# Kernel optimization log

Measured on AMD Instinct MI355X. Metric: run time of the kernel, lower is better.

## Reference

```python
import jax, jax.numpy as jnp
import numpy as np

N = 20        # number_of_nodes
K = 2         # Chebyshev order
E_DIM = 4     # embedding_dimensions
OUT = 2       # out_channels
F_IN = 8      # node_features
B = 131072    # batch


def setup_inputs() -> dict:
    key = jax.random.key(0)
    ks = jax.random.split(key, 8)
    x = jax.random.normal(ks[0], (B, N, F_IN), jnp.float32)
    e = jax.random.normal(ks[1], (N, E_DIM), jnp.float32)
    # AVWGCN parameter pools: weights_pool (E_DIM, K, in, out), bias_pool (E_DIM, out)
    gate_w = jax.random.normal(ks[2], (E_DIM, K, F_IN + OUT, 2 * OUT), jnp.float32) * 0.1
    gate_b = jax.random.normal(ks[3], (E_DIM, 2 * OUT), jnp.float32) * 0.1
    upd_w = jax.random.normal(ks[4], (E_DIM, K, F_IN + OUT, OUT), jnp.float32) * 0.1
    upd_b = jax.random.normal(ks[5], (E_DIM, OUT), jnp.float32) * 0.1
    lin_w = jax.random.normal(ks[6], (1, OUT), jnp.float32) * 0.5
    lin_b = jax.random.normal(ks[7], (1,), jnp.float32) * 0.1
    return {"x": x, "e": e, "gate_w": gate_w, "gate_b": gate_b,
            "upd_w": upd_w, "upd_b": upd_b, "lin_w": lin_w, "lin_b": lin_b}


def _avwgcn(x, e, supports, w_pool, b_pool):
    # Node-adaptive weights: (N, K, in, out) and bias (N, out)
    W = jnp.einsum('nd,dkio->nkio', e, w_pool)
    b = e @ b_pool
    # K-hop graph conv gather: (B, N, K, in)
    x_g = jnp.einsum('knm,bmc->bnkc', supports, x)
    return jnp.einsum('bnki,nkio->bno', x_g, W) + b


def reference(x, e, gate_w, gate_b, upd_w, upd_b, lin_w, lin_b):
    dt = x.dtype
    # Adaptive adjacency: softmax(relu(E E^T)) rows; Chebyshev set for K=2 is [I, A]
    A = jax.nn.softmax(jax.nn.relu(e @ e.T), axis=1)
    supports = jnp.stack([jnp.eye(N, dtype=dt), A.astype(dt)])  # (K, N, N)

    H = jnp.zeros((x.shape[0], N, OUT), dt)  # self.h is None -> zeros
    XH = jnp.concatenate([x, H], axis=-1)
    ZR = jax.nn.sigmoid(_avwgcn(XH, e, supports, gate_w, gate_b))
    Z, R = ZR[..., :OUT], ZR[..., OUT:]
    C = jnp.concatenate([x, Z * H], axis=-1)
    HC = jnp.tanh(_avwgcn(C, e, supports, upd_w, upd_b))
    H = R * H + (1.0 - R) * HC

    y = jax.nn.relu(H)
    y = y @ lin_w.T + lin_b
    return y
```

## Files before the change

kernel.cpp:

```cpp
#include <hip/hip_runtime.h>
#include <math.h>

#define NN 20
#define ED 4
#define XROW 160
#define NC 80
#define NKT 5
#define NNT 5
#define FRAG_BYTES (NKT * NNT * 64 * 16)
#define BIAS_OFF   FRAG_BYTES
#define LIN_OFF    (BIAS_OFF + NC * 4)
#define CONS_BYTES (LIN_OFF + 16)
#define CONS_U4    (CONS_BYTES / 16)
#define THREADS 512
#define STH 640
#define ROWS_PER_WAVE 16
#define ROWS_PER_BLOCK 128

typedef __attribute__((ext_vector_type(8))) _Float16 half8;
typedef __attribute__((ext_vector_type(4))) float f32x4;
typedef __attribute__((ext_vector_type(4))) unsigned uint4v;

static __device__ __forceinline__ half8 cvt8(float4 a, float4 b) {
    uint4v u = (uint4v){
        __builtin_bit_cast(unsigned, __builtin_amdgcn_cvt_pkrtz(a.x, a.y)),
        __builtin_bit_cast(unsigned, __builtin_amdgcn_cvt_pkrtz(a.z, a.w)),
        __builtin_bit_cast(unsigned, __builtin_amdgcn_cvt_pkrtz(b.x, b.y)),
        __builtin_bit_cast(unsigned, __builtin_amdgcn_cvt_pkrtz(b.z, b.w))};
    return __builtin_bit_cast(half8, u);
}

static __device__ __forceinline__ float dpp_xor1(float v) {
    return __builtin_bit_cast(float,
        __builtin_amdgcn_mov_dpp(__builtin_bit_cast(int, v), 0xB1, 0xF, 0xF, true));
}
static __device__ __forceinline__ float dpp_xor2(float v) {
    return __builtin_bit_cast(float,
        __builtin_amdgcn_mov_dpp(__builtin_bit_cast(int, v), 0x4E, 0xF, 0xF, true));
}

__global__ __launch_bounds__(STH) void rgcn_setup(
        const float* __restrict__ e,
        const float* __restrict__ gate_w,
        const float* __restrict__ gate_b,
        const float* __restrict__ upd_w,
        const float* __restrict__ upd_b,
        const float* __restrict__ lin_w,
        const float* __restrict__ lin_b,
        char* __restrict__ ws) {
    __shared__ float el[80];
    __shared__ float sA[400];
    __shared__ float wself[640];
    __shared__ float wagg[640];
    const int t = threadIdx.x;
    const int l = t & 63;
    const int w = t >> 6;

    const int c = t >> 3, i = t & 7;
    const int n_ = c >> 2, ro = c & 3;
    float p0[4], p1[4];
    {
        const float* b0;
        const float* b1;
        int st;
        if (ro < 2) { b0 = gate_w + i * 4 + 2 + ro; b1 = b0 + 40; st = 80; }
        else        { b0 = upd_w  + i * 2 + ro - 2; b1 = b0 + 20; st = 40; }
        #pragma unroll
        for (int d = 0; d < ED; ++d) { p0[d] = b0[d * st]; p1[d] = b1[d * st]; }
    }
    float pb[4];
    if (t < NC) {
        int rb = t & 3;
        #pragma unroll
        for (int d = 0; d < ED; ++d)
            pb[d] = (rb < 2) ? gate_b[d * 4 + 2 + rb] : upd_b[d * 2 + rb - 2];
    }
    if (t < 80) el[t] = e[t];
    float* wbias = (float*)(ws + BIAS_OFF);
    float* wlin  = (float*)(ws + LIN_OFF);
    if (t == 0) { wlin[0] = lin_w[0]; wlin[1] = lin_w[1]; wlin[2] = lin_b[0]; wlin[3] = 0.f; }
    __syncthreads();

    if (t < 400) {
        int nn = t / 20, mm = t - (t / 20) * 20;
        float d = 0.f;
        for (int j = 0; j < ED; ++j) d += el[nn * ED + j] * el[mm * ED + j];
        sA[t] = fmaxf(d, 0.f);
    }
    {
        float vs = 0.f, va = 0.f;
        #pragma unroll
        for (int d = 0; d < ED; ++d) {
            float ev = el[n_ * ED + d];
            vs += ev * p0[d];
            va += ev * p1[d];
        }
        wself[t] = vs;
        wagg[t]  = va;
    }
    if (t < NC) {
        float b = 0.f;
        #pragma unroll
        for (int d = 0; d < ED; ++d) b += el[(t >> 2) * ED + d] * pb[d];
        wbias[t] = b;
    }
    __syncthreads();

    if (t < NN) {
        float mx = -1e30f;
        for (int m = 0; m < NN; ++m) mx = fmaxf(mx, sA[t * 20 + m]);
        float ex[NN]; float sum = 0.f;
        for (int m = 0; m < NN; ++m) { ex[m] = __expf(sA[t * 20 + m] - mx); sum += ex[m]; }
        float inv = 1.f / sum;
        for (int m = 0; m < NN; ++m) sA[t * 20 + m] = ex[m] * inv;
    }
    __syncthreads();

    half8* frag = (half8*)ws;
    for (int tile = w; tile < NKT * NNT; tile += (STH / 64)) {
        int kt = tile / 5, nt = tile - kt * 5;
        int cc = nt * 16 + (l & 15);
        int nn = cc >> 2;
        int mm = kt * 4 + (l >> 4);
        float anm = sA[nn * 20 + mm];
        float4 wg0 = *(const float4*)&wagg[cc * 8];
        float4 wg1 = *(const float4*)&wagg[cc * 8 + 4];
        float v0 = anm * wg0.x, v1 = anm * wg0.y, v2 = anm * wg0.z, v3 = anm * wg0.w;
        float v4 = anm * wg1.x, v5 = anm * wg1.y, v6 = anm * wg1.z, v7 = anm * wg1.w;
        if (nn == mm) {
            float4 ws0 = *(const float4*)&wself[cc * 8];
            float4 ws1 = *(const float4*)&wself[cc * 8 + 4];
            v0 += ws0.x; v1 += ws0.y; v2 += ws0.z; v3 += ws0.w;
            v4 += ws1.x; v5 += ws1.y; v6 += ws1.z; v7 += ws1.w;
        }
        half8 hv;
        hv[0] = (_Float16)v0; hv[1] = (_Float16)v1; hv[2] = (_Float16)v2; hv[3] = (_Float16)v3;
        hv[4] = (_Float16)v4; hv[5] = (_Float16)v5; hv[6] = (_Float16)v6; hv[7] = (_Float16)v7;
        frag[tile * 64 + l] = hv;
    }
}

__global__ __launch_bounds__(THREADS, 6) void rgcn_main(
        const float* __restrict__ x,
        const char* __restrict__ cons,
        float* __restrict__ y) {
    __shared__ __align__(16) char smem[CONS_BYTES];
    const int t = threadIdx.x;
    const int l = t & 63;
    const int w = t >> 6;

    const size_t row0 = (size_t)blockIdx.x * ROWS_PER_BLOCK + (size_t)w * ROWS_PER_WAVE;
    const float* xp = x + (row0 + (l & 15)) * XROW + ((l >> 4) << 3);
    float4 xa0 = *(const float4*)(xp);       float4 xb0 = *(const float4*)(xp + 4);
    float4 xa1 = *(const float4*)(xp + 32);  float4 xb1 = *(const float4*)(xp + 36);
    float4 xa2 = *(const float4*)(xp + 64);  float4 xb2 = *(const float4*)(xp + 68);
    float4 xa3 = *(const float4*)(xp + 96);  float4 xb3 = *(const float4*)(xp + 100);
    float4 xa4 = *(const float4*)(xp + 128); float4 xb4 = *(const float4*)(xp + 132);

    {
        const uint4v* src = (const uint4v*)cons;
        uint4v* dst = (uint4v*)smem;
        #pragma unroll
        for (int i = t; i < CONS_U4; i += THREADS) dst[i] = src[i];
    }
    __syncthreads();

    const half8* frag = (const half8*)smem;
    const float* sbias = (const float*)(smem + BIAS_OFF);
    const float* slin  = (const float*)(smem + LIN_OFF);

    f32x4 acc[NNT];
    #pragma unroll
    for (int nt = 0; nt < NNT; ++nt) {
        float b = sbias[nt * 16 + (l & 15)];
        acc[nt] = (f32x4){b, b, b, b};
    }

    #define STEP(XA, XB, KT)                                                        \
    {                                                                               \
        half8 a = cvt8(XA, XB);                                                     \
        _Pragma("unroll")                                                           \
        for (int nt = 0; nt < NNT; ++nt) {                                          \
            half8 bh = frag[((KT) * NNT + nt) * 64 + l];                            \
            acc[nt] = __builtin_amdgcn_mfma_f32_16x16x32_f16(a, bh, acc[nt], 0, 0, 0); \
        }                                                                           \
    }
    STEP(xa0, xb0, 0)
    STEP(xa1, xb1, 1)
    STEP(xa2, xb2, 2)
    STEP(xa3, xb3, 3)
    STEP(xa4, xb4, 4)
    #undef STEP

    const float lw0 = slin[0], lw1 = slin[1], lb = slin[2];
    const int ro = l & 3;
    const bool isR = ro < 2;
    const float myw = (ro & 1) ? lw1 : lw0;
    const size_t rowb = row0 + ((l >> 4) << 2) + ro;

    #pragma unroll
    for (int nt = 0; nt < NNT; ++nt) {
        const int n = nt * 4 + ((l & 15) >> 2);
        float ysel = 0.f;
        #pragma unroll
        for (int q = 0; q < 4; ++q) {
            float pre = acc[nt][q];
            float term;
            if (isR) {
                term = __builtin_amdgcn_rcpf(1.f + __expf(pre));
            } else {
                term = 1.f - 2.f * __builtin_amdgcn_rcpf(__expf(2.f * pre) + 1.f);
            }
            float other = dpp_xor2(term);
            float h = term * other;
            float s = fmaxf(h, 0.f) * myw;
            float yq = s + dpp_xor1(s) + lb;
            if (q == ro) ysel = yq;
        }
        y[rowb * NN + n] = ysel;
    }
}

extern "C" void kernel_launch(void* const* d_in, const int* in_sizes, int n_in,
                              void* d_out, int out_size, void* d_ws, size_t ws_size,
                              hipStream_t stream) {
    const float* x      = (const float*)d_in[0];
    const float* e      = (const float*)d_in[1];
    const float* gate_w = (const float*)d_in[2];
    const float* gate_b = (const float*)d_in[3];
    const float* upd_w  = (const float*)d_in[4];
    const float* upd_b  = (const float*)d_in[5];
    const float* lin_w  = (const float*)d_in[6];
    const float* lin_b  = (const float*)d_in[7];
    char* cons = (char*)d_ws;
    float* y   = (float*)d_out;

    const int Bn = in_sizes[0] / XROW;
    const int nblocks = Bn / ROWS_PER_BLOCK;

    rgcn_setup<<<1, STH, 0, stream>>>(e, gate_w, gate_b, upd_w, upd_b,
                                      lin_w, lin_b, cons);
    rgcn_main<<<nblocks, THREADS, 0, stream>>>(x, cons, y);
}
```

Baseline: 26.90 us.

## Fuse weight setup into main kernel, recomputing constants per block

```diff
diff --git a/kernel.cpp b/kernel.cpp
--- a/kernel.cpp
+++ b/kernel.cpp
@@ -8,12 +8,7 @@
 #define NKT 5
 #define NNT 5
 #define FRAG_BYTES (NKT * NNT * 64 * 16)
-#define BIAS_OFF   FRAG_BYTES
-#define LIN_OFF    (BIAS_OFF + NC * 4)
-#define CONS_BYTES (LIN_OFF + 16)
-#define CONS_U4    (CONS_BYTES / 16)
 #define THREADS 512
-#define STH 640
 #define ROWS_PER_WAVE 16
 #define ROWS_PER_BLOCK 128
 
@@ -39,7 +34,8 @@
         __builtin_amdgcn_mov_dpp(__builtin_bit_cast(int, v), 0x4E, 0xF, 0xF, true));
 }
 
-__global__ __launch_bounds__(STH) void rgcn_setup(
+__global__ __launch_bounds__(THREADS, 4) void rgcn_fused(
+        const float* __restrict__ x,
         const float* __restrict__ e,
         const float* __restrict__ gate_w,
         const float* __restrict__ gate_b,
@@ -47,62 +43,61 @@
         const float* __restrict__ upd_b,
         const float* __restrict__ lin_w,
         const float* __restrict__ lin_b,
-        char* __restrict__ ws) {
+        float* __restrict__ y) {
+    __shared__ __align__(16) char fragmem[FRAG_BYTES];
+    __shared__ float sbias[NC];
     __shared__ float el[80];
     __shared__ float sA[400];
     __shared__ float wself[640];
     __shared__ float wagg[640];
+
     const int t = threadIdx.x;
     const int l = t & 63;
     const int w = t >> 6;
 
-    const int c = t >> 3, i = t & 7;
-    const int n_ = c >> 2, ro = c & 3;
-    float p0[4], p1[4];
-    {
-        const float* b0;
-        const float* b1;
-        int st;
-        if (ro < 2) { b0 = gate_w + i * 4 + 2 + ro; b1 = b0 + 40; st = 80; }
-        else        { b0 = upd_w  + i * 2 + ro - 2; b1 = b0 + 20; st = 40; }
-        #pragma unroll
-        for (int d = 0; d < ED; ++d) { p0[d] = b0[d * st]; p1[d] = b1[d * st]; }
-    }
-    float pb[4];
-    if (t < NC) {
-        int rb = t & 3;
-        #pragma unroll
-        for (int d = 0; d < ED; ++d)
-            pb[d] = (rb < 2) ? gate_b[d * 4 + 2 + rb] : upd_b[d * 2 + rb - 2];
-    }
-    if (t < 80) el[t] = e[t];
-    float* wbias = (float*)(ws + BIAS_OFF);
-    float* wlin  = (float*)(ws + LIN_OFF);
-    if (t == 0) { wlin[0] = lin_w[0]; wlin[1] = lin_w[1]; wlin[2] = lin_b[0]; wlin[3] = 0.f; }
+    const size_t row0 = (size_t)blockIdx.x * ROWS_PER_BLOCK + (size_t)w * ROWS_PER_WAVE;
+    const float* xp = x + (row0 + (l & 15)) * XROW + ((l >> 4) << 3);
+    float4 xa0 = *(const float4*)(xp);       float4 xb0 = *(const float4*)(xp + 4);
+    float4 xa1 = *(const float4*)(xp + 32);  float4 xb1 = *(const float4*)(xp + 36);
+    float4 xa2 = *(const float4*)(xp + 64);  float4 xb2 = *(const float4*)(xp + 68);
+    float4 xa3 = *(const float4*)(xp + 96);  float4 xb3 = *(const float4*)(xp + 100);
+    float4 xa4 = *(const float4*)(xp + 128); float4 xb4 = *(const float4*)(xp + 132);
+
+    if (t < NN * ED) el[t] = e[t];
     __syncthreads();
 
     if (t < 400) {
         int nn = t / 20, mm = t - (t / 20) * 20;
         float d = 0.f;
+        #pragma unroll
         for (int j = 0; j < ED; ++j) d += el[nn * ED + j] * el[mm * ED + j];
         sA[t] = fmaxf(d, 0.f);
     }
-    {
-        float vs = 0.f, va = 0.f;
-        #pragma unroll
-        for (int d = 0; d < ED; ++d) {
-            float ev = el[n_ * ED + d];
-            vs += ev * p0[d];
-            va += ev * p1[d];
+    #pragma unroll
+    for (int idx = t; idx < 1280; idx += THREADS) {
+        int sel = idx >= 640;
+        int rem = sel ? idx - 640 : idx;
+        int c = rem >> 3, i = rem & 7;
+        int n = c >> 2, ro = c & 3;
+        float v = 0.f;
+        if (ro < 2) {
+            int o = 2 + ro;
+            #pragma unroll
+            for (int d = 0; d < ED; ++d) v += el[n * ED + d] * gate_w[d * 80 + sel * 40 + i * 4 + o];
+        } else {
+            int o = ro - 2;
+            #pragma unroll
+            for (int d = 0; d < ED; ++d) v += el[n * ED + d] * upd_w[d * 40 + sel * 20 + i * 2 + o];
         }
-        wself[t] = vs;
-        wagg[t]  = va;
+        (sel ? wagg : wself)[rem] = v;
     }
     if (t < NC) {
+        int n = t >> 2, ro = t & 3;
         float b = 0.f;
         #pragma unroll
-        for (int d = 0; d < ED; ++d) b += el[(t >> 2) * ED + d] * pb[d];
-        wbias[t] = b;
+        for (int d = 0; d < ED; ++d)
+            b += el[n * ED + d] * (ro < 2 ? gate_b[d * 4 + 2 + ro] : upd_b[d * 2 + ro - 2]);
+        sbias[t] = b;
     }
     __syncthreads();
 
@@ -116,59 +111,33 @@
     }
     __syncthreads();
 
-    half8* frag = (half8*)ws;
-    for (int tile = w; tile < NKT * NNT; tile += (STH / 64)) {
-        int kt = tile / 5, nt = tile - kt * 5;
-        int cc = nt * 16 + (l & 15);
-        int nn = cc >> 2;
-        int mm = kt * 4 + (l >> 4);
-        float anm = sA[nn * 20 + mm];
-        float4 wg0 = *(const float4*)&wagg[cc * 8];
-        float4 wg1 = *(const float4*)&wagg[cc * 8 + 4];
-        float v0 = anm * wg0.x, v1 = anm * wg0.y, v2 = anm * wg0.z, v3 = anm * wg0.w;
-        float v4 = anm * wg1.x, v5 = anm * wg1.y, v6 = anm * wg1.z, v7 = anm * wg1.w;
-        if (nn == mm) {
-            float4 ws0 = *(const float4*)&wself[cc * 8];
-            float4 ws1 = *(const float4*)&wself[cc * 8 + 4];
-            v0 += ws0.x; v1 += ws0.y; v2 += ws0.z; v3 += ws0.w;
-            v4 += ws1.x; v5 += ws1.y; v6 += ws1.z; v7 += ws1.w;
+    {
+        half8* frag = (half8*)fragmem;
+        for (int tile = w; tile < NKT * NNT; tile += 8) {
+            int kt = tile / 5, nt = tile - kt * 5;
+            int cc = nt * 16 + (l & 15);
+            int nn = cc >> 2;
+            int mm = kt * 4 + (l >> 4);
+            float anm = sA[nn * 20 + mm];
+            float4 wg0 = *(const float4*)&wagg[cc * 8];
+            float4 wg1 = *(const float4*)&wagg[cc * 8 + 4];
+            float v0 = anm * wg0.x, v1 = anm * wg0.y, v2 = anm * wg0.z, v3 = anm * wg0.w;
+            float v4 = anm * wg1.x, v5 = anm * wg1.y, v6 = anm * wg1.z, v7 = anm * wg1.w;
+            if (nn == mm) {
+                float4 ws0 = *(const float4*)&wself[cc * 8];
+                float4 ws1 = *(const float4*)&wself[cc * 8 + 4];
+                v0 += ws0.x; v1 += ws0.y; v2 += ws0.z; v3 += ws0.w;
+                v4 += ws1.x; v5 += ws1.y; v6 += ws1.z; v7 += ws1.w;
+            }
+            half8 hv;
+            hv[0] = (_Float16)v0; hv[1] = (_Float16)v1; hv[2] = (_Float16)v2; hv[3] = (_Float16)v3;
+            hv[4] = (_Float16)v4; hv[5] = (_Float16)v5; hv[6] = (_Float16)v6; hv[7] = (_Float16)v7;
+            frag[tile * 64 + l] = hv;
         }
-        half8 hv;
-        hv[0] = (_Float16)v0; hv[1] = (_Float16)v1; hv[2] = (_Float16)v2; hv[3] = (_Float16)v3;
-        hv[4] = (_Float16)v4; hv[5] = (_Float16)v5; hv[6] = (_Float16)v6; hv[7] = (_Float16)v7;
-        frag[tile * 64 + l] = hv;
-    }
-}
-
-__global__ __launch_bounds__(THREADS, 6) void rgcn_main(
-        const float* __restrict__ x,
-        const char* __restrict__ cons,
-        float* __restrict__ y) {
-    __shared__ __align__(16) char smem[CONS_BYTES];
-    const int t = threadIdx.x;
-    const int l = t & 63;
-    const int w = t >> 6;
-
-    const size_t row0 = (size_t)blockIdx.x * ROWS_PER_BLOCK + (size_t)w * ROWS_PER_WAVE;
-    const float* xp = x + (row0 + (l & 15)) * XROW + ((l >> 4) << 3);
-    float4 xa0 = *(const float4*)(xp);       float4 xb0 = *(const float4*)(xp + 4);
-    float4 xa1 = *(const float4*)(xp + 32);  float4 xb1 = *(const float4*)(xp + 36);
-    float4 xa2 = *(const float4*)(xp + 64);  float4 xb2 = *(const float4*)(xp + 68);
-    float4 xa3 = *(const float4*)(xp + 96);  float4 xb3 = *(const float4*)(xp + 100);
-    float4 xa4 = *(const float4*)(xp + 128); float4 xb4 = *(const float4*)(xp + 132);
-
-    {
-        const uint4v* src = (const uint4v*)cons;
-        uint4v* dst = (uint4v*)smem;
-        #pragma unroll
-        for (int i = t; i < CONS_U4; i += THREADS) dst[i] = src[i];
-    }
-    __syncthreads();
-
-    const half8* frag = (const half8*)smem;
-    const float* sbias = (const float*)(smem + BIAS_OFF);
-    const float* slin  = (const float*)(smem + LIN_OFF);
-
+    }
+    __syncthreads();
+
+    const half8* frag = (const half8*)fragmem;
     f32x4 acc[NNT];
     #pragma unroll
     for (int nt = 0; nt < NNT; ++nt) {
@@ -192,7 +161,7 @@
     STEP(xa4, xb4, 4)
     #undef STEP
 
-    const float lw0 = slin[0], lw1 = slin[1], lb = slin[2];
+    const float lw0 = lin_w[0], lw1 = lin_w[1], lb = lin_b[0];
     const int ro = l & 3;
     const bool isR = ro < 2;
     const float myw = (ro & 1) ? lw1 : lw0;
@@ -232,13 +201,11 @@
     const float* upd_b  = (const float*)d_in[5];
     const float* lin_w  = (const float*)d_in[6];
     const float* lin_b  = (const float*)d_in[7];
-    char* cons = (char*)d_ws;
-    float* y   = (float*)d_out;
+    float* y = (float*)d_out;
 
     const int Bn = in_sizes[0] / XROW;
     const int nblocks = Bn / ROWS_PER_BLOCK;
 
-    rgcn_setup<<<1, STH, 0, stream>>>(e, gate_w, gate_b, upd_w, upd_b,
-                                      lin_w, lin_b, cons);
-    rgcn_main<<<nblocks, THREADS, 0, stream>>>(x, cons, y);
-}
+    rgcn_fused<<<nblocks, THREADS, 0, stream>>>(x, e, gate_w, gate_b,
+                                                upd_w, upd_b, lin_w, lin_b, y);
+}
```

Result: no change. 26.55 us (-1.3%).
